# Kernel tuning notes

Measured on AMD Instinct MI355X. Metric: run time of the kernel, lower is better.

The kernel has to match this reference:

```python
import jax, jax.numpy as jnp
import numpy as np

B, S, D_IN, H, L = 32, 1024, 128, 256, 2
ND = 2  # bidirectional


def setup_inputs() -> dict:
    key = jax.random.key(0)
    ks = iter(jax.random.split(key, 40))

    def p(shape, scale=0.05):
        return jax.random.normal(next(ks), shape, dtype=jnp.float32) * scale

    inp = {"x": jax.random.normal(next(ks), (B, S, D_IN), dtype=jnp.float32)}
    dims_in = [D_IN, H * ND]
    for l in range(L):
        for tag in ("f", "b"):
            inp[f"w_ih_l{l}{tag}"] = p((4 * H, dims_in[l]))
            inp[f"w_hh_l{l}{tag}"] = p((4 * H, H))
            inp[f"b_l{l}{tag}"] = p((4 * H,))  # b_ih + b_hh fused (identical math)
    inp["attn_w"] = p((H * ND,))   # nn.Linear(2H, 1) weight
    inp["attn_b"] = p((1,))
    inp["head_w"] = p((D_IN, H * ND))  # forecasting head: Linear(2H, input_dim)
    inp["head_b"] = p((D_IN,))
    return inp


def _lstm_dir(x, w_ih, w_hh, b, reverse):
    """Single-direction LSTM over [B,S,F] -> [B,S,H]. PyTorch gate order i,f,g,o."""
    Bb = x.shape[0]
    Hh = w_hh.shape[1]
    # Precompute input projections once: [S,B,4H]
    xp = jnp.einsum('bsi,gi->sbg', x, w_ih) + b
    if reverse:
        xp = xp[::-1]
    h0 = jnp.zeros((Bb, Hh), x.dtype)
    c0 = jnp.zeros((Bb, Hh), x.dtype)

    def step(carry, gx):
        h, c = carry
        g = gx + h @ w_hh.T
        i, f, gg, o = jnp.split(g, 4, axis=-1)
        c = jax.nn.sigmoid(f) * c + jax.nn.sigmoid(i) * jnp.tanh(gg)
        h = jax.nn.sigmoid(o) * jnp.tanh(c)
        return (h, c), h

    _, hs = jax.lax.scan(step, (h0, c0), xp)
    if reverse:
        hs = hs[::-1]
    return jnp.swapaxes(hs, 0, 1)  # [B,S,H]


def reference(x,
              w_ih_l0f, w_hh_l0f, b_l0f, w_ih_l0b, w_hh_l0b, b_l0b,
              w_ih_l1f, w_hh_l1f, b_l1f, w_ih_l1b, w_hh_l1b, b_l1b,
              attn_w, attn_b, head_w, head_b):
    h = x
    layers = [((w_ih_l0f, w_hh_l0f, b_l0f), (w_ih_l0b, w_hh_l0b, b_l0b)),
              ((w_ih_l1f, w_hh_l1f, b_l1f), (w_ih_l1b, w_hh_l1b, b_l1b))]
    for fw, bw in layers:
        hf = _lstm_dir(h, *fw, False)
        hb = _lstm_dir(h, *bw, True)
        h = jnp.concatenate([hf, hb], axis=-1)  # [B,S,2H]; dropout off (eval)
    # Prefix attention pooling: original recomputes softmax over output[:, :i+1]
    # for every i. Equivalently (softmax is shift-invariant per prefix):
    # context_i = cumsum(e * h)_i / cumsum(e)_i with e = exp(s - max(s)).
    s = h @ attn_w + attn_b[0]                      # [B,S] attention scores
    e = jnp.exp(s - jnp.max(s, axis=1, keepdims=True))
    num = jnp.cumsum(e[..., None] * h, axis=1)      # [B,S,2H]
    den = jnp.cumsum(e, axis=1)[..., None]          # [B,S,1]
    context = num / den                             # [B,S,2H]
    forecasts = context @ head_w.T + head_b         # [B,S,D_IN]
    return forecasts
```

## Files before the change

kernel.cpp:

```cpp
#include <hip/hip_runtime.h>

typedef unsigned short ushort_t;
typedef unsigned int uint_t;
typedef unsigned long long u64;
typedef __attribute__((ext_vector_type(8))) short short8;
typedef __attribute__((ext_vector_type(4))) float floatx4;

#define S_LEN 1024
#define BATCH 32
#define HDIM  256
#define GDIM  1024
#define DIN   128
#define SALT  0x00C0FFEE00000000ULL

__device__ __forceinline__ float bf2f(ushort_t u) { return __uint_as_float(((unsigned)u) << 16); }
__device__ __forceinline__ float bf2fs(short s)   { return __uint_as_float(((unsigned)(unsigned short)s) << 16); }
__device__ __forceinline__ ushort_t f2bf(float f) {
  unsigned u = __float_as_uint(f);
  unsigned r = (u + 0x7fffu + ((u >> 16) & 1u)) >> 16;
  return (ushort_t)r;
}
__device__ __forceinline__ float sigf(float x) { return 1.f / (1.f + __expf(-x)); }
__device__ __forceinline__ float tanh_f(float x) {
  float ax = fabsf(x);
  float e = __expf(2.f * ax);
  float r = 1.f - 2.f / (e + 1.f);
  return x < 0.f ? -r : r;
}

__device__ __forceinline__ void load_lds16(const void* g, void* l) {
  __builtin_amdgcn_global_load_lds((const __attribute__((address_space(1))) unsigned int*)g,
                                   (__attribute__((address_space(3))) unsigned int*)l, 16, 0, 0);
}
__device__ __forceinline__ void vm0() { asm volatile("s_waitcnt vmcnt(0)" ::: "memory"); }

__global__ __launch_bounds__(256) void gemm_bf16(
    const ushort_t* __restrict__ A, const ushort_t* __restrict__ Bw,
    const float* __restrict__ bias, void* __restrict__ Cout,
    int M, int N, int K, int mode)
{
  __shared__ __align__(16) ushort_t As[128 * 64];
  __shared__ __align__(16) ushort_t Bs[128 * 64];
  const int tid = threadIdx.x;
  const int lane = tid & 63, wid = tid >> 6;
  const int wm = wid >> 1, wn = wid & 1;
  const int bm = blockIdx.y, bn = blockIdx.x;
  const int l15 = lane & 15, q4 = lane >> 4;

  const int r  = tid >> 3;
  const int c8 = tid & 7;
  const int g8 = c8 ^ (r & 7);

  floatx4 zero4 = {0.f, 0.f, 0.f, 0.f};
  floatx4 acc[4][4];
#pragma unroll
  for (int mt = 0; mt < 4; ++mt)
#pragma unroll
    for (int nt = 0; nt < 4; ++nt) acc[mt][nt] = zero4;

  for (int k0 = 0; k0 < K; k0 += 64) {
    __syncthreads();
#pragma unroll
    for (int p = 0; p < 4; ++p) {
      int row = p * 32 + r;
      load_lds16(A + (size_t)(bm * 128 + row) * K + k0 + g8 * 8, (void*)(As + p * 2048 + wid * 512));
      load_lds16(Bw + (size_t)(bn * 128 + row) * K + k0 + g8 * 8, (void*)(Bs + p * 2048 + wid * 512));
    }
    __syncthreads();
#pragma unroll
    for (int ks = 0; ks < 2; ++ks) {
      const int kk = ks * 4 + q4;
      short8 af[4], bf[4];
#pragma unroll
      for (int mt = 0; mt < 4; ++mt) {
        int row = wm * 64 + mt * 16 + l15;
        af[mt] = *(const short8*)(As + row * 64 + ((kk ^ (row & 7)) << 3));
      }
#pragma unroll
      for (int nt = 0; nt < 4; ++nt) {
        int row = wn * 64 + nt * 16 + l15;
        bf[nt] = *(const short8*)(Bs + row * 64 + ((kk ^ (row & 7)) << 3));
      }
#pragma unroll
      for (int mt = 0; mt < 4; ++mt)
#pragma unroll
        for (int nt = 0; nt < 4; ++nt)
          acc[mt][nt] = __builtin_amdgcn_mfma_f32_16x16x32_bf16(af[mt], bf[nt], acc[mt][nt], 0, 0, 0);
    }
  }

#pragma unroll
  for (int mt = 0; mt < 4; ++mt)
#pragma unroll
    for (int nt = 0; nt < 4; ++nt)
#pragma unroll
      for (int rr = 0; rr < 4; ++rr) {
        int m = bm * 128 + wm * 64 + mt * 16 + q4 * 4 + rr;
        int n = bn * 128 + wn * 64 + nt * 16 + l15;
        float v = acc[mt][nt][rr] + bias[n];
        if (mode == 0) {
          ((ushort_t*)Cout)[(size_t)m * N + n] = f2bf(v);
        } else if (mode == 1) {
          int t = m >> 5, b = m & 31;
          ((float*)Cout)[(size_t)b * (S_LEN * DIN) + t * DIN + n] = v;
        } else {
          int t = m >> 5, b = m & 31;
          ((ushort_t*)Cout)[(size_t)t * (N * 32) + n * 32 + b] = f2bf(v);
        }
      }
}

__global__ __launch_bounds__(256) void lstm_layer(
    const ushort_t* __restrict__ xpf, const ushort_t* __restrict__ xpb,
    const ushort_t* __restrict__ whhf, const ushort_t* __restrict__ whhb,
    ushort_t* __restrict__ hout, u64* __restrict__ comm, u64* __restrict__ epochs)
{
  const int bx = blockIdx.x;
  const int dir = bx & 1, j = bx >> 1;

  const ushort_t* xp  = dir ? xpb : xpf;
  const ushort_t* whh = dir ? whhb : whhf;
  u64* commd = comm + (size_t)dir * 4096;
  const int hoff = dir * 256;

  __shared__ __align__(16) ushort_t hbuf[32 * 264];
  __shared__ __align__(16) float stage[32 * 132];

  const int tid = threadIdx.x, lane = tid & 63, w = tid >> 6;
  const int l15 = lane & 15, q4 = lane >> 4;

  short8 Bf[2][8];
#pragma unroll
  for (int tl = 0; tl < 2; ++tl) {
    int grow = w * 256 + j * 32 + tl * 16 + l15;
#pragma unroll
    for (int ks = 0; ks < 8; ++ks)
      Bf[tl][ks] = *(const short8*)(whh + (size_t)grow * 256 + ks * 32 + q4 * 8);
  }

  for (int i = tid; i < 32 * 132; i += 256) ((uint_t*)hbuf)[i] = 0u;

  float cst[4] = {0.f, 0.f, 0.f, 0.f};

  u64 xr64[2][2];
  auto ldxp = [&](int tt) {
#pragma unroll
    for (int mt = 0; mt < 2; ++mt)
#pragma unroll
      for (int tl = 0; tl < 2; ++tl) {
        int g = w * 256 + j * 32 + tl * 16 + l15;
        xr64[mt][tl] = *(const u64*)(xp + (size_t)tt * (GDIM * BATCH) + (size_t)g * 32 + mt * 16 + q4 * 4);
      }
  };

  const int cb  = tid >> 3;
  const int cg0 = tid & 7;
  const int bb  = tid >> 3;
  const int c4  = (tid & 7) * 4;

  ldxp((dir == 0) ? 0 : 1023);
  __syncthreads();

  for (int sc = 0; sc < 1024; ++sc) {
    const int tcur  = (dir == 0) ? sc : 1023 - sc;
    const int tnext = (dir == 0) ? (sc < 1023 ? sc + 1 : 1023) : (sc < 1023 ? 1022 - sc : 0);

    floatx4 acc[2][2];
#pragma unroll
    for (int mt = 0; mt < 2; ++mt)
#pragma unroll
      for (int tl = 0; tl < 2; ++tl) {
        u64 v = xr64[mt][tl];
#pragma unroll
        for (int rr = 0; rr < 4; ++rr)
          acc[mt][tl][rr] = bf2f((ushort_t)(v >> (16 * rr)));
      }

    ldxp(tnext);

    if (sc > 0) {
      if (w == 0) {
        const u64 want = SALT | (u64)(unsigned)sc;
        const u64* ea = epochs + ((size_t)(dir * 2 + (sc & 1)) * 8 + (lane & 7)) * 16;
        for (;;) {
          u64 v = __hip_atomic_load(ea, __ATOMIC_RELAXED, __HIP_MEMORY_SCOPE_AGENT);
          if (__ballot(v == want) == ~0ULL) break;
        }
      }
      __syncthreads();
      const u64* rbuf = commd + (size_t)(sc & 1) * 2048 + (size_t)cb * 64 + cg0 * 8;
      u64 tmp[8];
#pragma unroll
      for (int k = 0; k < 8; ++k)
        tmp[k] = __hip_atomic_load(rbuf + k, __ATOMIC_RELAXED, __HIP_MEMORY_SCOPE_AGENT);
#pragma unroll
      for (int k = 0; k < 8; ++k)
        *(u64*)(hbuf + cb * 264 + cg0 * 32 + k * 4) = tmp[k];
    }
    __syncthreads();

#pragma unroll
    for (int ks = 0; ks < 8; ++ks) {
      short8 a0 = *(const short8*)(hbuf + l15 * 264 + ks * 32 + q4 * 8);
      short8 a1 = *(const short8*)(hbuf + (16 + l15) * 264 + ks * 32 + q4 * 8);
      acc[0][0] = __builtin_amdgcn_mfma_f32_16x16x32_bf16(a0, Bf[0][ks], acc[0][0], 0, 0, 0);
      acc[0][1] = __builtin_amdgcn_mfma_f32_16x16x32_bf16(a0, Bf[1][ks], acc[0][1], 0, 0, 0);
      acc[1][0] = __builtin_amdgcn_mfma_f32_16x16x32_bf16(a1, Bf[0][ks], acc[1][0], 0, 0, 0);
      acc[1][1] = __builtin_amdgcn_mfma_f32_16x16x32_bf16(a1, Bf[1][ks], acc[1][1], 0, 0, 0);
    }

#pragma unroll
    for (int mt = 0; mt < 2; ++mt)
#pragma unroll
      for (int tl = 0; tl < 2; ++tl)
#pragma unroll
        for (int rr = 0; rr < 4; ++rr)
          stage[(mt * 16 + q4 * 4 + rr) * 132 + w * 32 + tl * 16 + l15] = acc[mt][tl][rr];
    __syncthreads();

    float hv4[4];
#pragma unroll
    for (int i = 0; i < 4; ++i) {
      float gi = stage[bb * 132 +       c4 + i];
      float gf = stage[bb * 132 + 32  + c4 + i];
      float gg = stage[bb * 132 + 64  + c4 + i];
      float go = stage[bb * 132 + 96  + c4 + i];
      float c = sigf(gf) * cst[i] + sigf(gi) * tanh_f(gg);
      cst[i] = c;
      hv4[i] = sigf(go) * tanh_f(c);
    }
    u64 pv = (u64)f2bf(hv4[0]) | ((u64)f2bf(hv4[1]) << 16) |
             ((u64)f2bf(hv4[2]) << 32) | ((u64)f2bf(hv4[3]) << 48);

    __hip_atomic_store(commd + (size_t)((sc + 1) & 1) * 2048 + (size_t)bb * 64 + j * 8 + (tid & 7),
                       pv, __ATOMIC_RELAXED, __HIP_MEMORY_SCOPE_AGENT);
    *(u64*)(hout + (size_t)tcur * (BATCH * 512) + bb * 512 + hoff + j * 32 + c4) = pv;
    vm0();
    __syncthreads();
    if (tid == 0)
      __hip_atomic_store(epochs + ((size_t)(dir * 2 + ((sc + 1) & 1)) * 8 + j) * 16,
                         SALT | (u64)(unsigned)(sc + 1), __ATOMIC_RELAXED, __HIP_MEMORY_SCOPE_AGENT);
  }
}

__global__ __launch_bounds__(256) void attn_scores(
    const ushort_t* __restrict__ h1, const float* __restrict__ attn_w,
    const float* __restrict__ attn_b, float* __restrict__ e_out)
{
  const int b = blockIdx.x;
  __shared__ float sbuf[1024];
  __shared__ float red[4];
  const int tid = threadIdx.x, lane = tid & 63, w = tid >> 6;

  float wreg[8];
#pragma unroll
  for (int i = 0; i < 8; ++i) wreg[i] = attn_w[lane * 8 + i];

  for (int t = w; t < 1024; t += 4) {
    short8 hv = *(const short8*)(h1 + (size_t)t * (BATCH * 512) + b * 512 + lane * 8);
    float dot = 0.f;
#pragma unroll
    for (int i = 0; i < 8; ++i) dot += bf2fs(hv[i]) * wreg[i];
#pragma unroll
    for (int off = 32; off; off >>= 1) dot += __shfl_xor(dot, off);
    if (lane == 0) sbuf[t] = dot + attn_b[0];
  }
  __syncthreads();
  float m = -1e30f;
  for (int t = tid; t < 1024; t += 256) m = fmaxf(m, sbuf[t]);
#pragma unroll
  for (int off = 32; off; off >>= 1) m = fmaxf(m, __shfl_xor(m, off));
  if (lane == 0) red[w] = m;
  __syncthreads();
  float mm = fmaxf(fmaxf(red[0], red[1]), fmaxf(red[2], red[3]));
  for (int t = tid; t < 1024; t += 256) e_out[b * 1024 + t] = __expf(sbuf[t] - mm);
}

__global__ __launch_bounds__(256) void attn_ctx(
    const ushort_t* __restrict__ h1, const float* __restrict__ e_in, ushort_t* __restrict__ ctx)
{
  const int b = blockIdx.x >> 1, half = blockIdx.x & 1;
  const int c = half * 256 + threadIdx.x;
  float num = 0.f, den = 0.f;
  const ushort_t* hp = h1 + b * 512 + c;
  ushort_t* cp = ctx + b * 512 + c;
  const float* ep = e_in + b * 1024;
#pragma unroll 4
  for (int t = 0; t < 1024; ++t) {
    float ev = ep[t];
    float hv = bf2f(hp[(size_t)t * (BATCH * 512)]);
    num += ev * hv;
    den += ev;
    cp[(size_t)t * (BATCH * 512)] = f2bf(num / den);
  }
}

__global__ void castw(const float* __restrict__ in, ushort_t* __restrict__ out, int n) {
  int i = blockIdx.x * 256 + threadIdx.x;
  if (i < n) out[i] = f2bf(in[i]);
}
__global__ void castx(const float* __restrict__ x, ushort_t* __restrict__ xt) {
  int i = blockIdx.x * 256 + threadIdx.x;
  int dcol = i & 127;
  int m = i >> 7;
  int b = m & 31, s = m >> 5;
  xt[i] = f2bf(x[(size_t)b * (S_LEN * DIN) + s * DIN + dcol]);
}

extern "C" void kernel_launch(void* const* d_in, const int* in_sizes, int n_in,
                              void* d_out, int out_size, void* d_ws, size_t ws_size,
                              hipStream_t stream)
{
  const float* x     = (const float*)d_in[0];
  const float* wih0f = (const float*)d_in[1];
  const float* whh0f = (const float*)d_in[2];
  const float* b0f   = (const float*)d_in[3];
  const float* wih0b = (const float*)d_in[4];
  const float* whh0b = (const float*)d_in[5];
  const float* b0b   = (const float*)d_in[6];
  const float* wih1f = (const float*)d_in[7];
  const float* whh1f = (const float*)d_in[8];
  const float* b1f   = (const float*)d_in[9];
  const float* wih1b = (const float*)d_in[10];
  const float* whh1b = (const float*)d_in[11];
  const float* b1b   = (const float*)d_in[12];
  const float* attw  = (const float*)d_in[13];
  const float* attb  = (const float*)d_in[14];
  const float* headw = (const float*)d_in[15];
  const float* headb = (const float*)d_in[16];
  float* out = (float*)d_out;

  char* p = (char*)d_ws;
  auto alloc = [&](size_t bytes) {
    char* r = p;
    p += (bytes + 511) & ~(size_t)511;
    return r;
  };
  u64* ep0        = (u64*)alloc(512 * 8);
  u64* ep1        = (u64*)alloc(512 * 8);
  u64* comm0      = (u64*)alloc(8192 * 8);
  u64* comm1      = (u64*)alloc(8192 * 8);
  ushort_t* xt    = (ushort_t*)alloc((size_t)32768 * 128 * 2);
  ushort_t* cwih0f = (ushort_t*)alloc(131072 * 2);
  ushort_t* cwih0b = (ushort_t*)alloc(131072 * 2);
  ushort_t* cwhh0f = (ushort_t*)alloc(262144 * 2);
  ushort_t* cwhh0b = (ushort_t*)alloc(262144 * 2);
  ushort_t* cwih1f = (ushort_t*)alloc(524288 * 2);
  ushort_t* cwih1b = (ushort_t*)alloc(524288 * 2);
  ushort_t* cwhh1f = (ushort_t*)alloc(262144 * 2);
  ushort_t* cwhh1b = (ushort_t*)alloc(262144 * 2);
  ushort_t* cwhead = (ushort_t*)alloc(65536 * 2);
  ushort_t* xpA = (ushort_t*)alloc((size_t)32768 * 1024 * 2);
  ushort_t* xpB = (ushort_t*)alloc((size_t)32768 * 1024 * 2);
  ushort_t* h0  = (ushort_t*)alloc((size_t)32768 * 512 * 2);
  ushort_t* h1  = (ushort_t*)alloc((size_t)32768 * 512 * 2);
  float* ebuf   = (float*)alloc(32 * 1024 * 4);
  ushort_t* ctx = xpA;

  (void)in_sizes; (void)n_in; (void)out_size; (void)ws_size;

  (void)hipMemsetAsync(ep0, 0, 2 * 512 * 8, stream);

  castw<<<512, 256, 0, stream>>>(wih0f, cwih0f, 131072);
  castw<<<512, 256, 0, stream>>>(wih0b, cwih0b, 131072);
  castw<<<1024, 256, 0, stream>>>(whh0f, cwhh0f, 262144);
  castw<<<1024, 256, 0, stream>>>(whh0b, cwhh0b, 262144);
  castw<<<2048, 256, 0, stream>>>(wih1f, cwih1f, 524288);
  castw<<<2048, 256, 0, stream>>>(wih1b, cwih1b, 524288);
  castw<<<1024, 256, 0, stream>>>(whh1f, cwhh1f, 262144);
  castw<<<1024, 256, 0, stream>>>(whh1b, cwhh1b, 262144);
  castw<<<256, 256, 0, stream>>>(headw, cwhead, 65536);
  castx<<<16384, 256, 0, stream>>>(x, xt);

  gemm_bf16<<<dim3(8, 256), 256, 0, stream>>>(xt, cwih0f, b0f, xpA, 32768, 1024, 128, 2);
  gemm_bf16<<<dim3(8, 256), 256, 0, stream>>>(xt, cwih0b, b0b, xpB, 32768, 1024, 128, 2);
  lstm_layer<<<16, 256, 0, stream>>>(xpA, xpB, cwhh0f, cwhh0b, h0, comm0, ep0);

  gemm_bf16<<<dim3(8, 256), 256, 0, stream>>>(h0, cwih1f, b1f, xpA, 32768, 1024, 512, 2);
  gemm_bf16<<<dim3(8, 256), 256, 0, stream>>>(h0, cwih1b, b1b, xpB, 32768, 1024, 512, 2);
  lstm_layer<<<16, 256, 0, stream>>>(xpA, xpB, cwhh1f, cwhh1b, h1, comm1, ep1);

  attn_scores<<<32, 256, 0, stream>>>(h1, attw, attb, ebuf);
  attn_ctx<<<64, 256, 0, stream>>>(h1, ebuf, ctx);
  gemm_bf16<<<dim3(1, 256), 256, 0, stream>>>(ctx, cwhead, headb, out, 32768, 128, 512, 1);
}
```

Measured before the change: 7.735 ms.

## Replace epoch flags with per-word tagged payloads in LSTM cross-block exchange

Each hidden-state word exchanged between blocks now carries a step tag in its upper 32 bits. Consumers spin directly on the payload words until every tag matches, instead of polling separate epoch flags. This removes the producer's vmcnt wait, the extra barrier and the flag store, and the consumer's separate flag poll, which shortens the per-timestep critical path of the serial recurrence. In exchange the communication buffer doubles in size and each consumer polls 16 words per step rather than one flag.

```diff
diff --git a/kernel.cpp b/kernel.cpp
--- a/kernel.cpp
+++ b/kernel.cpp
@@ -11,7 +11,7 @@
 #define HDIM  256
 #define GDIM  1024
 #define DIN   128
-#define SALT  0x00C0FFEE00000000ULL
+#define TAG_BASE 0xC0FFE000u
 
 __device__ __forceinline__ float bf2f(ushort_t u) { return __uint_as_float(((unsigned)u) << 16); }
 __device__ __forceinline__ float bf2fs(short s)   { return __uint_as_float(((unsigned)(unsigned short)s) << 16); }
@@ -32,7 +32,6 @@
   __builtin_amdgcn_global_load_lds((const __attribute__((address_space(1))) unsigned int*)g,
                                    (__attribute__((address_space(3))) unsigned int*)l, 16, 0, 0);
 }
-__device__ __forceinline__ void vm0() { asm volatile("s_waitcnt vmcnt(0)" ::: "memory"); }
 
 __global__ __launch_bounds__(256) void gemm_bf16(
     const ushort_t* __restrict__ A, const ushort_t* __restrict__ Bw,
@@ -113,14 +112,14 @@
 __global__ __launch_bounds__(256) void lstm_layer(
     const ushort_t* __restrict__ xpf, const ushort_t* __restrict__ xpb,
     const ushort_t* __restrict__ whhf, const ushort_t* __restrict__ whhb,
-    ushort_t* __restrict__ hout, u64* __restrict__ comm, u64* __restrict__ epochs)
+    ushort_t* __restrict__ hout, u64* __restrict__ comm)
 {
   const int bx = blockIdx.x;
   const int dir = bx & 1, j = bx >> 1;
 
   const ushort_t* xp  = dir ? xpb : xpf;
   const ushort_t* whh = dir ? whhb : whhf;
-  u64* commd = comm + (size_t)dir * 4096;
+  u64* commd = comm + (size_t)dir * 8192;
   const int hoff = dir * 256;
 
   __shared__ __align__(16) ushort_t hbuf[32 * 264];
@@ -179,23 +178,23 @@
     ldxp(tnext);
 
     if (sc > 0) {
-      if (w == 0) {
-        const u64 want = SALT | (u64)(unsigned)sc;
-        const u64* ea = epochs + ((size_t)(dir * 2 + (sc & 1)) * 8 + (lane & 7)) * 16;
-        for (;;) {
-          u64 v = __hip_atomic_load(ea, __ATOMIC_RELAXED, __HIP_MEMORY_SCOPE_AGENT);
-          if (__ballot(v == want) == ~0ULL) break;
-        }
-      }
-      __syncthreads();
-      const u64* rbuf = commd + (size_t)(sc & 1) * 2048 + (size_t)cb * 64 + cg0 * 8;
-      u64 tmp[8];
-#pragma unroll
-      for (int k = 0; k < 8; ++k)
-        tmp[k] = __hip_atomic_load(rbuf + k, __ATOMIC_RELAXED, __HIP_MEMORY_SCOPE_AGENT);
-#pragma unroll
-      for (int k = 0; k < 8; ++k)
-        *(u64*)(hbuf + cb * 264 + cg0 * 32 + k * 4) = tmp[k];
+      const unsigned want = TAG_BASE + (unsigned)sc;
+      const u64* rbuf = commd + (size_t)(sc & 1) * 4096 + (size_t)cb * 128 + cg0 * 16;
+      u64 v[16];
+      for (;;) {
+#pragma unroll
+        for (int k = 0; k < 16; ++k)
+          v[k] = __hip_atomic_load(rbuf + k, __ATOMIC_RELAXED, __HIP_MEMORY_SCOPE_AGENT);
+        unsigned bad = 0;
+#pragma unroll
+        for (int k = 0; k < 16; ++k) bad |= ((unsigned)(v[k] >> 32)) ^ want;
+        if (bad == 0) break;
+      }
+#pragma unroll
+      for (int k2 = 0; k2 < 8; ++k2) {
+        u64 d = (u64)(uint_t)v[2 * k2] | ((u64)(uint_t)v[2 * k2 + 1] << 32);
+        *(u64*)(hbuf + cb * 264 + cg0 * 32 + k2 * 4) = d;
+      }
     }
     __syncthreads();
 
@@ -232,14 +231,15 @@
     u64 pv = (u64)f2bf(hv4[0]) | ((u64)f2bf(hv4[1]) << 16) |
              ((u64)f2bf(hv4[2]) << 32) | ((u64)f2bf(hv4[3]) << 48);
 
-    __hip_atomic_store(commd + (size_t)((sc + 1) & 1) * 2048 + (size_t)bb * 64 + j * 8 + (tid & 7),
-                       pv, __ATOMIC_RELAXED, __HIP_MEMORY_SCOPE_AGENT);
-    *(u64*)(hout + (size_t)tcur * (BATCH * 512) + bb * 512 + hoff + j * 32 + c4) = pv;
-    vm0();
-    __syncthreads();
-    if (tid == 0)
-      __hip_atomic_store(epochs + ((size_t)(dir * 2 + ((sc + 1) & 1)) * 8 + j) * 16,
-                         SALT | (u64)(unsigned)(sc + 1), __ATOMIC_RELAXED, __HIP_MEMORY_SCOPE_AGENT);
+    {
+      u64* wbuf = commd + (size_t)((sc + 1) & 1) * 4096;
+      const u64 tagw = ((u64)(TAG_BASE + (unsigned)(sc + 1))) << 32;
+      size_t wi = (size_t)bb * 128 + j * 16 + (c4 >> 1);
+      __hip_atomic_store(wbuf + wi,     tagw | (uint_t)pv,         __ATOMIC_RELAXED, __HIP_MEMORY_SCOPE_AGENT);
+      __hip_atomic_store(wbuf + wi + 1, tagw | (uint_t)(pv >> 32), __ATOMIC_RELAXED, __HIP_MEMORY_SCOPE_AGENT);
+      *(u64*)(hout + (size_t)tcur * (BATCH * 512) + bb * 512 + hoff + j * 32 + c4) = pv;
+    }
+    __syncthreads();
   }
 }
 
@@ -336,10 +336,8 @@
     p += (bytes + 511) & ~(size_t)511;
     return r;
   };
-  u64* ep0        = (u64*)alloc(512 * 8);
-  u64* ep1        = (u64*)alloc(512 * 8);
-  u64* comm0      = (u64*)alloc(8192 * 8);
-  u64* comm1      = (u64*)alloc(8192 * 8);
+  u64* comm0      = (u64*)alloc(16384 * 8);
+  u64* comm1      = (u64*)alloc(16384 * 8);
   ushort_t* xt    = (ushort_t*)alloc((size_t)32768 * 128 * 2);
   ushort_t* cwih0f = (ushort_t*)alloc(131072 * 2);
   ushort_t* cwih0b = (ushort_t*)alloc(131072 * 2);
@@ -359,7 +357,7 @@
 
   (void)in_sizes; (void)n_in; (void)out_size; (void)ws_size;
 
-  (void)hipMemsetAsync(ep0, 0, 2 * 512 * 8, stream);
+  (void)hipMemsetAsync(comm0, 0, 2 * 16384 * 8, stream);
 
   castw<<<512, 256, 0, stream>>>(wih0f, cwih0f, 131072);
   castw<<<512, 256, 0, stream>>>(wih0b, cwih0b, 131072);
@@ -374,11 +372,11 @@
 
   gemm_bf16<<<dim3(8, 256), 256, 0, stream>>>(xt, cwih0f, b0f, xpA, 32768, 1024, 128, 2);
   gemm_bf16<<<dim3(8, 256), 256, 0, stream>>>(xt, cwih0b, b0b, xpB, 32768, 1024, 128, 2);
-  lstm_layer<<<16, 256, 0, stream>>>(xpA, xpB, cwhh0f, cwhh0b, h0, comm0, ep0);
+  lstm_layer<<<16, 256, 0, stream>>>(xpA, xpB, cwhh0f, cwhh0b, h0, comm0);
 
   gemm_bf16<<<dim3(8, 256), 256, 0, stream>>>(h0, cwih1f, b1f, xpA, 32768, 1024, 512, 2);
   gemm_bf16<<<dim3(8, 256), 256, 0, stream>>>(h0, cwih1b, b1b, xpB, 32768, 1024, 512, 2);
-  lstm_layer<<<16, 256, 0, stream>>>(xpA, xpB, cwhh1f, cwhh1b, h1, comm1, ep1);
+  lstm_layer<<<16, 256, 0, stream>>>(xpA, xpB, cwhh1f, cwhh1b, h1, comm1);
 
   attn_scores<<<32, 256, 0, stream>>>(h1, attw, attb, ebuf);
   attn_ctx<<<64, 256, 0, stream>>>(h1, ebuf, ctx);
```

New measurement: 9.355 ms. 20.9% more time.
